# Performance work log

Measured on AMD Instinct MI355X. Metric: run time of the kernel, lower is better.

Reference implementation:

```python
import jax, jax.numpy as jnp
import numpy as np

B, L, E, D, H, N_ENT = 64, 50, 50, 100, 100, 200000


def setup_inputs() -> dict:
    key = jax.random.key(0)
    ks = jax.random.split(key, 12)
    neighbor_ids = jax.random.randint(ks[0], (B, L, E), 0, N_ENT)
    # 0/1 adjacency; mimic GraphConstructer: symmetric with self-loops
    adj = jax.random.randint(ks[1], (B, L, E, E), 0, 2).astype(jnp.int32)
    adj = jnp.maximum(adj, adj.transpose(0, 1, 3, 2))
    adj = jnp.maximum(adj, jnp.eye(E, dtype=jnp.int32))
    s = 0.1  # ~ 1/sqrt(D) init scale
    emb = jax.random.normal(ks[2], (N_ENT, D), jnp.float32) * s
    Wq = jax.random.normal(ks[3], (D, H), jnp.float32) * s
    bq = jax.random.normal(ks[4], (H,), jnp.float32) * s
    Wk = jax.random.normal(ks[5], (D, H), jnp.float32) * s
    bk = jax.random.normal(ks[6], (H,), jnp.float32) * s
    Wv = jax.random.normal(ks[7], (D, H), jnp.float32) * s
    bv = jax.random.normal(ks[8], (H,), jnp.float32) * s
    Ws = jax.random.normal(ks[9], (D, H), jnp.float32) * s
    bs = jax.random.normal(ks[10], (H,), jnp.float32) * s
    return {"neighbor_ids": neighbor_ids, "adj": adj, "emb": emb,
            "Wq": Wq, "bq": bq, "Wk": Wk, "bk": bk,
            "Wv": Wv, "bv": bv, "Ws": Ws, "bs": bs}


def reference(neighbor_ids, adj, emb, Wq, bq, Wk, bk, Wv, bv, Ws, bs):
    b, l, e = neighbor_ids.shape
    d = emb.shape[1]
    h = Wq.shape[1]
    # embedding gather: [B,L,E,D] -> [G,E,D], G = B*L graphs
    x = emb[neighbor_ids].reshape(b * l, e, d)
    a = adj.reshape(b * l, e, e)
    # TransformerConv (heads=1): q,k,v linear with bias
    q = x @ Wq + bq
    k = x @ Wk + bk
    v = x @ Wv + bv
    scores = jnp.einsum('gid,gjd->gij', q, k) / jnp.sqrt(jnp.asarray(h, x.dtype))
    # edge (j -> i) exists when adj[j, i] != 0; target i attends over sources j
    mask = a.transpose(0, 2, 1) != 0  # mask[g, i, j]
    neg = jnp.finfo(scores.dtype).min
    attn = jax.nn.softmax(jnp.where(mask, scores, neg), axis=-1)
    # nodes with no incoming edge aggregate to zero (PyG softmax/scatter semantics)
    attn = jnp.where(mask.any(-1, keepdims=True), attn, jnp.zeros((), attn.dtype))
    agg = jnp.einsum('gij,gjd->gid', attn, v)
    out = agg + x @ Ws + bs  # root/skip connection with bias
    # take center node (index 0) of each ego-graph -> [B, L, H]
    return out.reshape(b, l, e, h)[:, :, 0, :]
```

## Files before the change

kernel.cpp:

```cpp
#include <hip/hip_runtime.h>
#include <hip/hip_bf16.h>
#include <math.h>

#define E_N 50
#define D_N 100
#define H_N 100

__device__ __forceinline__ float bf2f(unsigned int s16) {
    return __uint_as_float(s16 << 16);
}

__device__ __forceinline__ unsigned short f2bf(float f) {
    unsigned int u = __float_as_uint(f);
    unsigned int r = (u + 0x7FFFu + ((u >> 16) & 1u)) >> 16;
    return (unsigned short)r;
}

template <bool F32>
__device__ __forceinline__ float ldx(const void* p, int i) {
    if (F32) return reinterpret_cast<const float*>(p)[i];
    return bf2f(reinterpret_cast<const unsigned short*>(p)[i]);
}

template <bool F32>
__device__ __forceinline__ float4 ld4(const void* p, long long i4) {
    if (F32) return reinterpret_cast<const float4*>(p)[i4];
    uint2 v = reinterpret_cast<const uint2*>(p)[i4];
    float4 f;
    f.x = bf2f(v.x & 0xFFFFu);
    f.y = bf2f(v.x >> 16);
    f.z = bf2f(v.y & 0xFFFFu);
    f.w = bf2f(v.y >> 16);
    return f;
}

template <bool F32>
__device__ __forceinline__ void graph_core(
    int g, int tid,
    const int* __restrict__ nbr, const int* __restrict__ adj,
    const void* __restrict__ emb,
    const void* __restrict__ Wq, const void* __restrict__ bq,
    const void* __restrict__ Wk, const void* __restrict__ Wv,
    const void* __restrict__ bv, const void* __restrict__ Ws,
    const void* __restrict__ bs, void* __restrict__ out,
    float* xs, int* ids, int* msk, float* q0s, float* us,
    float* ssc, float* attns, float* ys, float* den_s)
{
    if (tid < E_N) {
        ids[tid] = nbr[g * E_N + tid];
        msk[tid] = adj[(size_t)g * (E_N * E_N) + tid * E_N];
    }
    __syncthreads();

    {
        const int total = E_N * (D_N / 4);
        for (int i = tid; i < total; i += 256) {
            int j  = i / 25;
            int d4 = i - j * 25;
            long long base4 = (long long)ids[j] * (D_N / 4) + d4;
            reinterpret_cast<float4*>(xs)[j * 25 + d4] = ld4<F32>(emb, base4);
        }
    }
    __syncthreads();

    if (tid < H_N) {
        float acc = ldx<F32>(bq, tid);
        for (int d = 0; d < D_N; ++d)
            acc = fmaf(xs[d], ldx<F32>(Wq, d * H_N + tid), acc);
        q0s[tid] = acc;
    }
    __syncthreads();

    if (tid < D_N) {
        float acc = 0.f;
        for (int h = 0; h < H_N; ++h)
            acc = fmaf(ldx<F32>(Wk, tid * H_N + h), q0s[h], acc);
        us[tid] = acc;
    }
    __syncthreads();

    if (tid < E_N) {
        float acc = 0.f;
        const float* xrow = xs + tid * D_N;
        for (int d = 0; d < D_N; ++d)
            acc = fmaf(us[d], xrow[d], acc);
        ssc[tid] = acc * 0.1f;
    }
    __syncthreads();

    float m = -3.0e38f;
    for (int j = 0; j < E_N; ++j)
        if (msk[j]) m = fmaxf(m, ssc[j]);
    if (tid < E_N)
        attns[tid] = msk[tid] ? __expf(ssc[tid] - m) : 0.f;
    __syncthreads();

    if (tid < D_N) {
        float den = 0.f;
        for (int j = 0; j < E_N; ++j) den += attns[j];
        float inv = den > 0.f ? 1.0f / den : 0.f;
        float acc = 0.f;
        for (int j = 0; j < E_N; ++j)
            acc = fmaf(attns[j], xs[j * D_N + tid], acc);
        ys[tid] = acc * inv;
        if (tid == 0) *den_s = den;
    }
    __syncthreads();

    if (tid < H_N) {
        float sflag = *den_s > 0.f ? 1.f : 0.f;
        float acc = ldx<F32>(bs, tid) + ldx<F32>(bv, tid) * sflag;
        for (int d = 0; d < D_N; ++d) {
            acc = fmaf(ys[d], ldx<F32>(Wv, d * H_N + tid), acc);
            acc = fmaf(xs[d], ldx<F32>(Ws, d * H_N + tid), acc);
        }
        size_t o = (size_t)g * H_N + tid;
        if (F32) reinterpret_cast<float*>(out)[o] = acc;
        else     reinterpret_cast<unsigned short*>(out)[o] = f2bf(acc);
    }
}

__global__ __launch_bounds__(256)
void graph_enc_kernel(const int* __restrict__ nbr,
                      const int* __restrict__ adj,
                      const void* __restrict__ emb,
                      const void* __restrict__ Wq, const void* __restrict__ bq,
                      const void* __restrict__ Wk, const void* __restrict__ Wv,
                      const void* __restrict__ bv, const void* __restrict__ Ws,
                      const void* __restrict__ bs, void* __restrict__ out)
{
    const int g = blockIdx.x;
    const int tid = threadIdx.x;

    __shared__ float xs[E_N * D_N];
    __shared__ int   ids[E_N];
    __shared__ int   msk[E_N];
    __shared__ float q0s[H_N];
    __shared__ float us[D_N];
    __shared__ float ssc[E_N];
    __shared__ float attns[E_N];
    __shared__ float ys[D_N];
    __shared__ float den_s;
    __shared__ int   is_f32_s;

    if (tid < 64) {
        unsigned short hw = reinterpret_cast<const unsigned short*>(emb)[tid * 2];
        float v = bf2f(hw);
        float a = fabsf(v);
        int sane = (v == 0.f) || (a >= 1e-4f && a <= 8.0f);
        unsigned long long ball = __ballot(sane);
        if (tid == 0) is_f32_s = (__popcll(ball) < 32) ? 1 : 0;
    }
    __syncthreads();

    if (is_f32_s)
        graph_core<true>(g, tid, nbr, adj, emb, Wq, bq, Wk, Wv, bv, Ws, bs, out,
                         xs, ids, msk, q0s, us, ssc, attns, ys, &den_s);
    else
        graph_core<false>(g, tid, nbr, adj, emb, Wq, bq, Wk, Wv, bv, Ws, bs, out,
                          xs, ids, msk, q0s, us, ssc, attns, ys, &den_s);
}

extern "C" void kernel_launch(void* const* d_in, const int* in_sizes, int n_in,
                              void* d_out, int out_size, void* d_ws, size_t ws_size,
                              hipStream_t stream) {
    const int* nbr = (const int*)d_in[0];
    const int* adj = (const int*)d_in[1];
    const void* emb = d_in[2];
    const void* Wq  = d_in[3];
    const void* bq  = d_in[4];
    const void* Wk  = d_in[5];
    const void* Wv  = d_in[7];
    const void* bv  = d_in[8];
    const void* Ws  = d_in[9];
    const void* bs  = d_in[10];

    const int G = in_sizes[0] / E_N;
    graph_enc_kernel<<<G, 256, 0, stream>>>(nbr, adj, emb, Wq, bq, Wk,
                                            Wv, bv, Ws, bs, d_out);
}
```

Baseline: 188.7 us.

## Transpose embedding tile in LDS, fuse softmax via wave shuffles, prefetch ids

The gathered embedding tile is stored transposed with a padded stride so the score, aggregation and projection loops read LDS without bank conflicts. The score, max, exp, sum and normalisation steps now run inside a single wavefront using shuffle reductions, which removes two barriers and the serial per-thread loops over all neighbours. Neighbour ids and mask values are loaded into registers before the format-detection barrier, overlapping their latency with it. The Wk dot product is vectorised with four accumulators. Launch bounds now request higher occupancy, which may add register pressure.

```diff
diff --git a/kernel.cpp b/kernel.cpp
--- a/kernel.cpp
+++ b/kernel.cpp
@@ -1,10 +1,12 @@
 #include <hip/hip_runtime.h>
-#include <hip/hip_bf16.h>
 #include <math.h>
 
 #define E_N 50
 #define D_N 100
 #define H_N 100
+#define XSTR 51
+#define NTHR 256
+#define GATHER_IT ((E_N * (D_N / 4) + NTHR - 1) / NTHR)
 
 __device__ __forceinline__ float bf2f(unsigned int s16) {
     return __uint_as_float(s16 << 16);
@@ -36,83 +38,95 @@
 
 template <bool F32>
 __device__ __forceinline__ void graph_core(
-    int g, int tid,
-    const int* __restrict__ nbr, const int* __restrict__ adj,
+    int g, int tid, int mk, const int* idr,
     const void* __restrict__ emb,
     const void* __restrict__ Wq, const void* __restrict__ bq,
     const void* __restrict__ Wk, const void* __restrict__ Wv,
     const void* __restrict__ bv, const void* __restrict__ Ws,
     const void* __restrict__ bs, void* __restrict__ out,
-    float* xs, int* ids, int* msk, float* q0s, float* us,
-    float* ssc, float* attns, float* ys, float* den_s)
+    float* xs, float* q0s, float* us, float* attns, float* ys, float* den_s)
 {
-    if (tid < E_N) {
-        ids[tid] = nbr[g * E_N + tid];
-        msk[tid] = adj[(size_t)g * (E_N * E_N) + tid * E_N];
-    }
-    __syncthreads();
-
-    {
-        const int total = E_N * (D_N / 4);
-        for (int i = tid; i < total; i += 256) {
+    #pragma unroll
+    for (int r = 0; r < GATHER_IT; ++r) {
+        int i = tid + NTHR * r;
+        if (i < E_N * (D_N / 4)) {
             int j  = i / 25;
             int d4 = i - j * 25;
-            long long base4 = (long long)ids[j] * (D_N / 4) + d4;
-            reinterpret_cast<float4*>(xs)[j * 25 + d4] = ld4<F32>(emb, base4);
+            float4 v = ld4<F32>(emb, (long long)idr[r] * (D_N / 4) + d4);
+            int d0 = d4 * 4;
+            xs[(d0 + 0) * XSTR + j] = v.x;
+            xs[(d0 + 1) * XSTR + j] = v.y;
+            xs[(d0 + 2) * XSTR + j] = v.z;
+            xs[(d0 + 3) * XSTR + j] = v.w;
         }
     }
     __syncthreads();
 
     if (tid < H_N) {
         float acc = ldx<F32>(bq, tid);
+        #pragma unroll 10
         for (int d = 0; d < D_N; ++d)
-            acc = fmaf(xs[d], ldx<F32>(Wq, d * H_N + tid), acc);
+            acc = fmaf(xs[d * XSTR], ldx<F32>(Wq, d * H_N + tid), acc);
         q0s[tid] = acc;
+    }
+    __syncthreads();
+
+    if (tid < D_N) {
+        float a0 = 0.f, a1 = 0.f, a2 = 0.f, a3 = 0.f;
+        const float4* q4 = reinterpret_cast<const float4*>(q0s);
+        #pragma unroll 5
+        for (int h4 = 0; h4 < H_N / 4; ++h4) {
+            float4 w = ld4<F32>(Wk, (long long)tid * (H_N / 4) + h4);
+            float4 q = q4[h4];
+            a0 = fmaf(w.x, q.x, a0);
+            a1 = fmaf(w.y, q.y, a1);
+            a2 = fmaf(w.z, q.z, a2);
+            a3 = fmaf(w.w, q.w, a3);
+        }
+        us[tid] = (a0 + a1) + (a2 + a3);
+    }
+    __syncthreads();
+
+    if (tid < 64) {
+        float s = 0.f;
+        if (tid < E_N) {
+            #pragma unroll 10
+            for (int d = 0; d < D_N; ++d)
+                s = fmaf(us[d], xs[d * XSTR + tid], s);
+            s *= 0.1f;
+        }
+        bool live = (tid < E_N) && (mk != 0);
+        float m = live ? s : -3.0e38f;
+        #pragma unroll
+        for (int off = 32; off; off >>= 1)
+            m = fmaxf(m, __shfl_xor(m, off));
+        float e = live ? __expf(s - m) : 0.f;
+        float den = e;
+        #pragma unroll
+        for (int off = 32; off; off >>= 1)
+            den += __shfl_xor(den, off);
+        float inv = den > 0.f ? 1.0f / den : 0.f;
+        if (tid < E_N) attns[tid] = e * inv;
+        if (tid == 0)  *den_s = den;
     }
     __syncthreads();
 
     if (tid < D_N) {
         float acc = 0.f;
-        for (int h = 0; h < H_N; ++h)
-            acc = fmaf(ldx<F32>(Wk, tid * H_N + h), q0s[h], acc);
-        us[tid] = acc;
-    }
-    __syncthreads();
-
-    if (tid < E_N) {
-        float acc = 0.f;
-        const float* xrow = xs + tid * D_N;
-        for (int d = 0; d < D_N; ++d)
-            acc = fmaf(us[d], xrow[d], acc);
-        ssc[tid] = acc * 0.1f;
-    }
-    __syncthreads();
-
-    float m = -3.0e38f;
-    for (int j = 0; j < E_N; ++j)
-        if (msk[j]) m = fmaxf(m, ssc[j]);
-    if (tid < E_N)
-        attns[tid] = msk[tid] ? __expf(ssc[tid] - m) : 0.f;
-    __syncthreads();
-
-    if (tid < D_N) {
-        float den = 0.f;
-        for (int j = 0; j < E_N; ++j) den += attns[j];
-        float inv = den > 0.f ? 1.0f / den : 0.f;
-        float acc = 0.f;
+        #pragma unroll 10
         for (int j = 0; j < E_N; ++j)
-            acc = fmaf(attns[j], xs[j * D_N + tid], acc);
-        ys[tid] = acc * inv;
-        if (tid == 0) *den_s = den;
+            acc = fmaf(attns[j], xs[tid * XSTR + j], acc);
+        ys[tid] = acc;
     }
     __syncthreads();
 
     if (tid < H_N) {
         float sflag = *den_s > 0.f ? 1.f : 0.f;
         float acc = ldx<F32>(bs, tid) + ldx<F32>(bv, tid) * sflag;
+        #pragma unroll 8
         for (int d = 0; d < D_N; ++d) {
-            acc = fmaf(ys[d], ldx<F32>(Wv, d * H_N + tid), acc);
-            acc = fmaf(xs[d], ldx<F32>(Ws, d * H_N + tid), acc);
+            acc = fmaf(ys[d],        ldx<F32>(Wv, d * H_N + tid), acc);
+            acc = fmaf(xs[d * XSTR], ldx<F32>(Ws, d * H_N + tid), acc);
         }
         size_t o = (size_t)g * H_N + tid;
         if (F32) reinterpret_cast<float*>(out)[o] = acc;
@@ -120,7 +134,7 @@
     }
 }
 
-__global__ __launch_bounds__(256)
+__global__ __launch_bounds__(NTHR, 7)
 void graph_enc_kernel(const int* __restrict__ nbr,
                       const int* __restrict__ adj,
                       const void* __restrict__ emb,
@@ -132,16 +146,23 @@
     const int g = blockIdx.x;
     const int tid = threadIdx.x;
 
-    __shared__ float xs[E_N * D_N];
-    __shared__ int   ids[E_N];
-    __shared__ int   msk[E_N];
-    __shared__ float q0s[H_N];
-    __shared__ float us[D_N];
-    __shared__ float ssc[E_N];
-    __shared__ float attns[E_N];
-    __shared__ float ys[D_N];
+    __shared__ __align__(16) float xs[D_N * XSTR];
+    __shared__ __align__(16) float q0s[H_N];
+    __shared__ __align__(16) float us[D_N];
+    __shared__ __align__(16) float attns[E_N];
+    __shared__ __align__(16) float ys[D_N];
     __shared__ float den_s;
     __shared__ int   is_f32_s;
+
+    int mk = 0;
+    if (tid < E_N) mk = adj[(size_t)g * (E_N * E_N) + tid * E_N];
+
+    int idr[GATHER_IT];
+    #pragma unroll
+    for (int r = 0; r < GATHER_IT; ++r) {
+        int i = tid + NTHR * r;
+        idr[r] = (i < E_N * (D_N / 4)) ? nbr[g * E_N + i / 25] : 0;
+    }
 
     if (tid < 64) {
         unsigned short hw = reinterpret_cast<const unsigned short*>(emb)[tid * 2];
@@ -154,11 +175,11 @@
     __syncthreads();
 
     if (is_f32_s)
-        graph_core<true>(g, tid, nbr, adj, emb, Wq, bq, Wk, Wv, bv, Ws, bs, out,
-                         xs, ids, msk, q0s, us, ssc, attns, ys, &den_s);
+        graph_core<true >(g, tid, mk, idr, emb, Wq, bq, Wk, Wv, bv, Ws, bs, out,
+                          xs, q0s, us, attns, ys, &den_s);
     else
-        graph_core<false>(g, tid, nbr, adj, emb, Wq, bq, Wk, Wv, bv, Ws, bs, out,
-                          xs, ids, msk, q0s, us, ssc, attns, ys, &den_s);
+        graph_core<false>(g, tid, mk, idr, emb, Wq, bq, Wk, Wv, bv, Ws, bs, out,
+                          xs, q0s, us, attns, ys, &den_s);
 }
 
 extern "C" void kernel_launch(void* const* d_in, const int* in_sizes, int n_in,
@@ -176,6 +197,6 @@
     const void* bs  = d_in[10];
 
     const int G = in_sizes[0] / E_N;
-    graph_enc_kernel<<<G, 256, 0, stream>>>(nbr, adj, emb, Wq, bq, Wk,
-                                            Wv, bv, Ws, bs, d_out);
-}
+    graph_enc_kernel<<<G, NTHR, 0, stream>>>(nbr, adj, emb, Wq, bq, Wk,
+                                             Wv, bv, Ws, bs, d_out);
+}
```

New measurement: 190.3 us. Within noise of the previous version (+0.9%).

## Precompute Wq·Wkᵀ product and batch four graphs per block

Applied to the files above, without the earlier changes.

Adds a precompute kernel that folds Wq and Wk into a D×D matrix and a bias vector, so each graph's key-side vector is a single matvec on the center embedding. The main kernel now handles four graphs per block and reuses each weight load across all four. It reads neighbor embeddings straight from global memory instead of staging the full x tile in shared memory, and skips masked neighbors during aggregation. The cost is a second kernel launch and more global gather traffic in the aggregation step.

```diff
diff --git a/kernel.cpp b/kernel.cpp
--- a/kernel.cpp
+++ b/kernel.cpp
@@ -1,10 +1,16 @@
 #include <hip/hip_runtime.h>
-#include <hip/hip_bf16.h>
 #include <math.h>
 
 #define E_N 50
 #define D_N 100
 #define H_N 100
+#define GPB 4
+#define NTHR 256
+#define SSP (E_N + 2)
+
+#define WS_AT 0
+#define WS_C  (D_N * D_N)
+#define WS_FLOATS (D_N * D_N + D_N)
 
 __device__ __forceinline__ float bf2f(unsigned int s16) {
     return __uint_as_float(s16 << 16);
@@ -34,131 +40,233 @@
     return f;
 }
 
-template <bool F32>
-__device__ __forceinline__ void graph_core(
-    int g, int tid,
-    const int* __restrict__ nbr, const int* __restrict__ adj,
-    const void* __restrict__ emb,
-    const void* __restrict__ Wq, const void* __restrict__ bq,
-    const void* __restrict__ Wk, const void* __restrict__ Wv,
-    const void* __restrict__ bv, const void* __restrict__ Ws,
-    const void* __restrict__ bs, void* __restrict__ out,
-    float* xs, int* ids, int* msk, float* q0s, float* us,
-    float* ssc, float* attns, float* ys, float* den_s)
-{
-    if (tid < E_N) {
-        ids[tid] = nbr[g * E_N + tid];
-        msk[tid] = adj[(size_t)g * (E_N * E_N) + tid * E_N];
-    }
-    __syncthreads();
-
-    {
-        const int total = E_N * (D_N / 4);
-        for (int i = tid; i < total; i += 256) {
-            int j  = i / 25;
-            int d4 = i - j * 25;
-            long long base4 = (long long)ids[j] * (D_N / 4) + d4;
-            reinterpret_cast<float4*>(xs)[j * 25 + d4] = ld4<F32>(emb, base4);
-        }
-    }
-    __syncthreads();
-
-    if (tid < H_N) {
-        float acc = ldx<F32>(bq, tid);
-        for (int d = 0; d < D_N; ++d)
-            acc = fmaf(xs[d], ldx<F32>(Wq, d * H_N + tid), acc);
-        q0s[tid] = acc;
-    }
-    __syncthreads();
-
-    if (tid < D_N) {
-        float acc = 0.f;
-        for (int h = 0; h < H_N; ++h)
-            acc = fmaf(ldx<F32>(Wk, tid * H_N + h), q0s[h], acc);
-        us[tid] = acc;
-    }
-    __syncthreads();
-
-    if (tid < E_N) {
-        float acc = 0.f;
-        const float* xrow = xs + tid * D_N;
-        for (int d = 0; d < D_N; ++d)
-            acc = fmaf(us[d], xrow[d], acc);
-        ssc[tid] = acc * 0.1f;
-    }
-    __syncthreads();
-
-    float m = -3.0e38f;
-    for (int j = 0; j < E_N; ++j)
-        if (msk[j]) m = fmaxf(m, ssc[j]);
-    if (tid < E_N)
-        attns[tid] = msk[tid] ? __expf(ssc[tid] - m) : 0.f;
-    __syncthreads();
-
-    if (tid < D_N) {
-        float den = 0.f;
-        for (int j = 0; j < E_N; ++j) den += attns[j];
-        float inv = den > 0.f ? 1.0f / den : 0.f;
-        float acc = 0.f;
-        for (int j = 0; j < E_N; ++j)
-            acc = fmaf(attns[j], xs[j * D_N + tid], acc);
-        ys[tid] = acc * inv;
-        if (tid == 0) *den_s = den;
-    }
-    __syncthreads();
-
-    if (tid < H_N) {
-        float sflag = *den_s > 0.f ? 1.f : 0.f;
-        float acc = ldx<F32>(bs, tid) + ldx<F32>(bv, tid) * sflag;
-        for (int d = 0; d < D_N; ++d) {
-            acc = fmaf(ys[d], ldx<F32>(Wv, d * H_N + tid), acc);
-            acc = fmaf(xs[d], ldx<F32>(Ws, d * H_N + tid), acc);
-        }
-        size_t o = (size_t)g * H_N + tid;
-        if (F32) reinterpret_cast<float*>(out)[o] = acc;
-        else     reinterpret_cast<unsigned short*>(out)[o] = f2bf(acc);
-    }
-}
-
-__global__ __launch_bounds__(256)
-void graph_enc_kernel(const int* __restrict__ nbr,
-                      const int* __restrict__ adj,
-                      const void* __restrict__ emb,
-                      const void* __restrict__ Wq, const void* __restrict__ bq,
-                      const void* __restrict__ Wk, const void* __restrict__ Wv,
-                      const void* __restrict__ bv, const void* __restrict__ Ws,
-                      const void* __restrict__ bs, void* __restrict__ out)
-{
-    const int g = blockIdx.x;
-    const int tid = threadIdx.x;
-
-    __shared__ float xs[E_N * D_N];
-    __shared__ int   ids[E_N];
-    __shared__ int   msk[E_N];
-    __shared__ float q0s[H_N];
-    __shared__ float us[D_N];
-    __shared__ float ssc[E_N];
-    __shared__ float attns[E_N];
-    __shared__ float ys[D_N];
-    __shared__ float den_s;
-    __shared__ int   is_f32_s;
-
+__device__ __forceinline__ int sniff_f32(const void* emb, int tid, int* slot) {
     if (tid < 64) {
         unsigned short hw = reinterpret_cast<const unsigned short*>(emb)[tid * 2];
         float v = bf2f(hw);
         float a = fabsf(v);
         int sane = (v == 0.f) || (a >= 1e-4f && a <= 8.0f);
         unsigned long long ball = __ballot(sane);
-        if (tid == 0) is_f32_s = (__popcll(ball) < 32) ? 1 : 0;
-    }
-    __syncthreads();
-
-    if (is_f32_s)
-        graph_core<true>(g, tid, nbr, adj, emb, Wq, bq, Wk, Wv, bv, Ws, bs, out,
-                         xs, ids, msk, q0s, us, ssc, attns, ys, &den_s);
+        if (tid == 0) *slot = (__popcll(ball) < 32) ? 1 : 0;
+    }
+    __syncthreads();
+    return *slot;
+}
+
+template <bool F32>
+__device__ __forceinline__ void precomp_core(
+    int dp, int tid, const void* __restrict__ Wq, const void* __restrict__ bq,
+    const void* __restrict__ Wk, float* __restrict__ ws, float* wq_s, float* bq_s)
+{
+    if (tid < H_N) wq_s[tid] = ldx<F32>(Wq, dp * H_N + tid);
+    if (dp == 0 && tid < H_N) bq_s[tid] = ldx<F32>(bq, tid);
+    __syncthreads();
+    if (tid < D_N) {
+        float a0 = 0.f, a1 = 0.f, a2 = 0.f, a3 = 0.f;
+        #pragma unroll
+        for (int h4 = 0; h4 < H_N / 4; ++h4) {
+            float4 w = ld4<F32>(Wk, (long long)tid * (H_N / 4) + h4);
+            a0 = fmaf(w.x, wq_s[h4 * 4 + 0], a0);
+            a1 = fmaf(w.y, wq_s[h4 * 4 + 1], a1);
+            a2 = fmaf(w.z, wq_s[h4 * 4 + 2], a2);
+            a3 = fmaf(w.w, wq_s[h4 * 4 + 3], a3);
+        }
+        ws[WS_AT + dp * D_N + tid] = (a0 + a1) + (a2 + a3);
+        if (dp == 0) {
+            float c0 = 0.f, c1 = 0.f, c2 = 0.f, c3 = 0.f;
+            #pragma unroll
+            for (int h4 = 0; h4 < H_N / 4; ++h4) {
+                float4 w = ld4<F32>(Wk, (long long)tid * (H_N / 4) + h4);
+                c0 = fmaf(w.x, bq_s[h4 * 4 + 0], c0);
+                c1 = fmaf(w.y, bq_s[h4 * 4 + 1], c1);
+                c2 = fmaf(w.z, bq_s[h4 * 4 + 2], c2);
+                c3 = fmaf(w.w, bq_s[h4 * 4 + 3], c3);
+            }
+            ws[WS_C + tid] = (c0 + c1) + (c2 + c3);
+        }
+    }
+}
+
+__global__ __launch_bounds__(128)
+void precomp_kernel(const void* __restrict__ Wq, const void* __restrict__ bq,
+                    const void* __restrict__ Wk, const void* __restrict__ emb,
+                    float* __restrict__ ws)
+{
+    __shared__ float wq_s[H_N];
+    __shared__ float bq_s[H_N];
+    __shared__ int is_f32_s;
+    int f32 = sniff_f32(emb, threadIdx.x, &is_f32_s);
+    if (f32) precomp_core<true >(blockIdx.x, threadIdx.x, Wq, bq, Wk, ws, wq_s, bq_s);
+    else     precomp_core<false>(blockIdx.x, threadIdx.x, Wq, bq, Wk, ws, wq_s, bq_s);
+}
+
+template <bool F32>
+__device__ __forceinline__ void graph_core(
+    int g0, int G, int tid,
+    const int* __restrict__ nbr, const int* __restrict__ adj,
+    const void* __restrict__ emb,
+    const void* __restrict__ Wv, const void* __restrict__ bv,
+    const void* __restrict__ Ws, const void* __restrict__ bs,
+    const float* __restrict__ ws, void* __restrict__ out,
+    float* x0s, float* wls, float* ss, float* es, float* ps,
+    float* ys, float* skc, int* ids_s, float* denf)
+{
+    int q_ = 0, j_ = 0, myid = 0, mymsk = 0;
+    if (tid < GPB * E_N) {
+        q_ = tid / E_N; j_ = tid - q_ * E_N;
+        int gq = g0 + q_; if (gq >= G) gq = G - 1;
+        myid = nbr[gq * E_N + j_];
+        ids_s[q_ * SSP + j_] = myid;
+        mymsk = adj[(size_t)gq * (E_N * E_N) + j_ * E_N];
+    }
+    if (tid < GPB * (D_N / 4)) {
+        int qq = tid / (D_N / 4), d4 = tid - qq * (D_N / 4);
+        int gq = g0 + qq; if (gq >= G) gq = G - 1;
+        int id0 = nbr[gq * E_N];
+        float4 v = ld4<F32>(emb, (long long)id0 * (D_N / 4) + d4);
+        reinterpret_cast<float4*>(x0s + qq * D_N)[d4] = v;
+    }
+    __syncthreads();
+
+    if (tid < D_N) {
+        float cv = ws[WS_C + tid];
+        float a0 = cv, a1 = cv, a2 = cv, a3 = cv;
+        #pragma unroll 4
+        for (int dp = 0; dp < D_N; ++dp) {
+            float a = ws[WS_AT + dp * D_N + tid];
+            a0 = fmaf(a, x0s[0 * D_N + dp], a0);
+            a1 = fmaf(a, x0s[1 * D_N + dp], a1);
+            a2 = fmaf(a, x0s[2 * D_N + dp], a2);
+            a3 = fmaf(a, x0s[3 * D_N + dp], a3);
+        }
+        wls[0 * D_N + tid] = a0; wls[1 * D_N + tid] = a1;
+        wls[2 * D_N + tid] = a2; wls[3 * D_N + tid] = a3;
+    } else if (tid >= 128 && tid < 128 + H_N) {
+        int h = tid - 128;
+        float s0 = 0.f, s1 = 0.f, s2 = 0.f, s3 = 0.f;
+        #pragma unroll 4
+        for (int d = 0; d < D_N; ++d) {
+            float w = ldx<F32>(Ws, d * H_N + h);
+            s0 = fmaf(w, x0s[0 * D_N + d], s0);
+            s1 = fmaf(w, x0s[1 * D_N + d], s1);
+            s2 = fmaf(w, x0s[2 * D_N + d], s2);
+            s3 = fmaf(w, x0s[3 * D_N + d], s3);
+        }
+        skc[0 * H_N + h] = s0; skc[1 * H_N + h] = s1;
+        skc[2 * H_N + h] = s2; skc[3 * H_N + h] = s3;
+    }
+    __syncthreads();
+
+    float s_reg = 0.f, e_reg = 0.f;
+    if (tid < GPB * E_N) {
+        const float* wv = wls + q_ * D_N;
+        float a0 = 0.f, a1 = 0.f, a2 = 0.f, a3 = 0.f;
+        #pragma unroll
+        for (int d4 = 0; d4 < D_N / 4; ++d4) {
+            float4 xv = ld4<F32>(emb, (long long)myid * (D_N / 4) + d4);
+            a0 = fmaf(xv.x, wv[4 * d4 + 0], a0);
+            a1 = fmaf(xv.y, wv[4 * d4 + 1], a1);
+            a2 = fmaf(xv.z, wv[4 * d4 + 2], a2);
+            a3 = fmaf(xv.w, wv[4 * d4 + 3], a3);
+        }
+        s_reg = ((a0 + a1) + (a2 + a3)) * 0.1f;
+        ss[q_ * SSP + j_] = mymsk ? s_reg : -3.0e38f;
+    }
+    __syncthreads();
+    if (tid < GPB * E_N) {
+        float m = -3.0e38f;
+        #pragma unroll
+        for (int j = 0; j < E_N; ++j) m = fmaxf(m, ss[q_ * SSP + j]);
+        e_reg = mymsk ? __expf(s_reg - m) : 0.f;
+        es[q_ * SSP + j_] = e_reg;
+    }
+    __syncthreads();
+    if (tid < GPB * E_N) {
+        float den = 0.f;
+        #pragma unroll
+        for (int j = 0; j < E_N; ++j) den += es[q_ * SSP + j];
+        float inv = den > 0.f ? 1.f / den : 0.f;
+        ps[q_ * SSP + j_] = e_reg * inv;
+        if (j_ == 0) denf[q_] = den;
+    }
+    __syncthreads();
+
+    #pragma unroll
+    for (int rep = 0; rep < 2; ++rep) {
+        int idx = tid + NTHR * rep;
+        if (idx < GPB * D_N) {
+            int q = idx / D_N, d = idx - q * D_N;
+            float acc = 0.f;
+            #pragma unroll 10
+            for (int j = 0; j < E_N; ++j) {
+                float p = ps[q * SSP + j];
+                if (p > 0.f) {
+                    int id = ids_s[q * SSP + j];
+                    acc = fmaf(p, ldx<F32>(emb, id * D_N + d), acc);
+                }
+            }
+            ys[q * D_N + d] = acc;
+        }
+    }
+    __syncthreads();
+
+    if (tid < H_N) {
+        float b   = ldx<F32>(bs, tid);
+        float bvv = ldx<F32>(bv, tid);
+        float a0 = b + (denf[0] > 0.f ? bvv : 0.f) + skc[0 * H_N + tid];
+        float a1 = b + (denf[1] > 0.f ? bvv : 0.f) + skc[1 * H_N + tid];
+        float a2 = b + (denf[2] > 0.f ? bvv : 0.f) + skc[2 * H_N + tid];
+        float a3 = b + (denf[3] > 0.f ? bvv : 0.f) + skc[3 * H_N + tid];
+        #pragma unroll 4
+        for (int d = 0; d < D_N; ++d) {
+            float w = ldx<F32>(Wv, d * H_N + tid);
+            a0 = fmaf(w, ys[0 * D_N + d], a0);
+            a1 = fmaf(w, ys[1 * D_N + d], a1);
+            a2 = fmaf(w, ys[2 * D_N + d], a2);
+            a3 = fmaf(w, ys[3 * D_N + d], a3);
+        }
+        float accs[GPB] = {a0, a1, a2, a3};
+        #pragma unroll
+        for (int q = 0; q < GPB; ++q) {
+            int gq = g0 + q;
+            if (gq < G) {
+                size_t o = (size_t)gq * H_N + tid;
+                if (F32) reinterpret_cast<float*>(out)[o] = accs[q];
+                else     reinterpret_cast<unsigned short*>(out)[o] = f2bf(accs[q]);
+            }
+        }
+    }
+}
+
+__global__ __launch_bounds__(NTHR, 4)
+void graph_enc_kernel(const int* __restrict__ nbr,
+                      const int* __restrict__ adj,
+                      const void* __restrict__ emb,
+                      const void* __restrict__ Wv, const void* __restrict__ bv,
+                      const void* __restrict__ Ws, const void* __restrict__ bs,
+                      const float* __restrict__ ws, void* __restrict__ out, int G)
+{
+    const int g0 = blockIdx.x * GPB;
+    const int tid = threadIdx.x;
+
+    __shared__ __align__(16) float x0s[GPB * D_N];
+    __shared__ __align__(16) float wls[GPB * D_N];
+    __shared__ __align__(16) float ss [GPB * SSP];
+    __shared__ __align__(16) float es [GPB * SSP];
+    __shared__ __align__(16) float ps [GPB * SSP];
+    __shared__ __align__(16) float ys [GPB * D_N];
+    __shared__ __align__(16) float skc[GPB * H_N];
+    __shared__ __align__(16) int   ids_s[GPB * SSP];
+    __shared__ float denf[GPB];
+    __shared__ int is_f32_s;
+
+    int f32 = sniff_f32(emb, tid, &is_f32_s);
+    if (f32)
+        graph_core<true >(g0, G, tid, nbr, adj, emb, Wv, bv, Ws, bs, ws, out,
+                          x0s, wls, ss, es, ps, ys, skc, ids_s, denf);
     else
-        graph_core<false>(g, tid, nbr, adj, emb, Wq, bq, Wk, Wv, bv, Ws, bs, out,
-                          xs, ids, msk, q0s, us, ssc, attns, ys, &den_s);
+        graph_core<false>(g0, G, tid, nbr, adj, emb, Wv, bv, Ws, bs, ws, out,
+                          x0s, wls, ss, es, ps, ys, skc, ids_s, denf);
 }
 
 extern "C" void kernel_launch(void* const* d_in, const int* in_sizes, int n_in,
@@ -175,7 +283,10 @@
     const void* Ws  = d_in[9];
     const void* bs  = d_in[10];
 
+    float* ws = (float*)d_ws;
     const int G = in_sizes[0] / E_N;
-    graph_enc_kernel<<<G, 256, 0, stream>>>(nbr, adj, emb, Wq, bq, Wk,
-                                            Wv, bv, Ws, bs, d_out);
-}
+
+    precomp_kernel<<<D_N, 128, 0, stream>>>(Wq, bq, Wk, emb, ws);
+    graph_enc_kernel<<<(G + GPB - 1) / GPB, NTHR, 0, stream>>>(
+        nbr, adj, emb, Wv, bv, Ws, bs, ws, d_out, G);
+}
```

After: 220.8 us. 1.17x slower.
